# Kernel optimization log

Measured on AMD Instinct MI355X. Metric: run time of the kernel, lower is better.

## Reference

```python
import jax, jax.numpy as jnp
import numpy as np

B, S, IN_DIM, CTX = 32, 512, 256, 128
D, H, L = 128, 4, 2
DH = D // H
HID = 512
TOTAL = 11 * D * D + 8 * D  # hypernet flat weight size per sample
EPS = 1e-5


def _layernorm(x, g, b):
    mu = jnp.mean(x, axis=-1, keepdims=True)
    var = jnp.mean(jnp.square(x - mu), axis=-1, keepdims=True)
    return (x - mu) * jax.lax.rsqrt(var + EPS) * g + b


def setup_inputs() -> dict:
    key = jax.random.key(0)
    ks = jax.random.split(key, 24)
    f32 = jnp.float32
    inp = {
        'x': jax.random.normal(ks[0], (B, S, IN_DIM), f32),
        'context_vector': jax.random.normal(ks[1], (B, CTX), f32),
        'in_proj_w': jax.random.normal(ks[2], (D, IN_DIM), f32) * (IN_DIM ** -0.5),
        'in_proj_b': jnp.zeros((D,), f32),
        'pe': jax.random.normal(ks[3], (1, S, D), f32) * 0.02,
        'hfc1_w': jax.random.normal(ks[4], (L, HID, CTX), f32) * (CTX ** -0.5),
        'hfc1_b': jnp.zeros((L, HID), f32),
        'hfc2_w': jax.random.normal(ks[5], (L, TOTAL, HID), f32) * 0.02,
        'hfc2_b': jnp.zeros((L, TOTAL), f32),
        'out_proj_w': jax.random.normal(ks[6], (L, D, D), f32) * (D ** -0.5),
        'out_proj_b': jnp.zeros((L, D), f32),
        'ln1_g': jnp.ones((L, D), f32), 'ln1_b': jnp.zeros((L, D), f32),
        'ln2_g': jnp.ones((L, D), f32), 'ln2_b': jnp.zeros((L, D), f32),
        'alpha1': jnp.full((L,), 0.5, f32), 'alpha2': jnp.full((L,), 0.5, f32),
        'head_w': jax.random.normal(ks[7], (1, D), f32) * (D ** -0.5),
        'head_b': jnp.zeros((1,), f32),
    }
    return inp


def reference(x, context_vector, in_proj_w, in_proj_b, pe, hfc1_w, hfc1_b,
              hfc2_w, hfc2_b, out_proj_w, out_proj_b, ln1_g, ln1_b,
              ln2_g, ln2_b, alpha1, alpha2, head_w, head_b):
    # input projection + learned positional encoding
    h = jnp.einsum('bsi,di->bsd', x, in_proj_w) + in_proj_b
    h = h + pe[:, :h.shape[1], :]

    # flat split offsets for hypernet output
    sizes = [3 * D * D, 3 * D, 4 * D * D, 4 * D, 4 * D * D, D]
    offs = np.concatenate([[0], np.cumsum(sizes)])

    for l in range(L):
        # hypernet: per-sample weights from context
        hid = jax.nn.relu(context_vector @ hfc1_w[l].T + hfc1_b[l])
        flat = hid @ hfc2_w[l].T + hfc2_b[l]  # [B, TOTAL]
        aw = flat[:, offs[0]:offs[1]].reshape(B, 3 * D, D)
        ab = flat[:, offs[1]:offs[2]]                     # [B, 3D]
        f1w = flat[:, offs[2]:offs[3]].reshape(B, 4 * D, D)
        f1b = flat[:, offs[3]:offs[4]]                    # [B, 4D]
        f2w = flat[:, offs[4]:offs[5]].reshape(B, D, 4 * D)
        f2b = flat[:, offs[5]:offs[6]]                    # [B, D]

        # per-sample QKV projection (grouped GEMM over batch)
        qkv = jnp.einsum('bsd,bed->bse', h, aw) + ab[:, None, :]
        q, k, v = jnp.split(qkv, 3, axis=-1)
        q = q.reshape(B, S, H, DH)
        k = k.reshape(B, S, H, DH)
        v = v.reshape(B, S, H, DH)
        scores = jnp.einsum('bqhd,bkhd->bhqk', q, k) / jnp.sqrt(jnp.float32(DH))
        attn = jax.nn.softmax(scores, axis=-1)
        ctx = jnp.einsum('bhqk,bkhd->bqhd', attn, v).reshape(B, S, D)
        attn_out = jnp.einsum('bsd,ed->bse', ctx, out_proj_w[l]) + out_proj_b[l]

        h = _layernorm(h + alpha1[l] * attn_out, ln1_g[l], ln1_b[l])

        # per-sample FFN
        ff = jax.nn.relu(jnp.einsum('bsd,bfd->bsf', h, f1w) + f1b[:, None, :])
        ff = jnp.einsum('bsf,bdf->bsd', ff, f2w) + f2b[:, None, :]

        h = _layernorm(h + alpha2[l] * ff, ln2_g[l], ln2_b[l])

    out = h[:, -1, :] @ head_w.T + head_b  # [B, 1]
    return out
```

## Files before the change

kernel.cpp:

```cpp
#include <hip/hip_runtime.h>
#include <hip/hip_bf16.h>

constexpr int B_    = 32;
constexpr int S_    = 512;
constexpr int INDIM = 256;
constexpr int KCTX  = 128;
constexpr int D_    = 128;
constexpr int H_    = 4;
constexpr int L_    = 2;
constexpr int HID_  = 512;
constexpr int TOTAL_ = 11 * D_ * D_ + 8 * D_;
constexpr int OFF_AB  = 3 * D_ * D_;
constexpr int OFF_F1W = OFF_AB + 3 * D_;
constexpr int OFF_F1B = OFF_F1W + 4 * D_ * D_;
constexpr int OFF_F2W = OFF_F1B + 4 * D_;
constexpr int OFF_F2B = OFF_F2W + 4 * D_ * D_;
constexpr int TP = 132;

typedef __attribute__((ext_vector_type(8))) short short8;
typedef __attribute__((ext_vector_type(4))) short short4v;
typedef __attribute__((ext_vector_type(2))) short short2v;
typedef __attribute__((ext_vector_type(4))) float f32x4;

#define MFMA16 __builtin_amdgcn_mfma_f32_16x16x32_bf16

__device__ __forceinline__ short f2bf(float f) {
  __hip_bfloat16 h = __float2bfloat16(f);
  return __builtin_bit_cast(short, h);
}
__device__ __forceinline__ float bf2f(short s) {
  __hip_bfloat16 h = __builtin_bit_cast(__hip_bfloat16, s);
  return __bfloat162float(h);
}
struct bfpair { short hi, lo; };
__device__ __forceinline__ bfpair split2p(float x) {
  bfpair p;
  p.hi = f2bf(x);
  p.lo = f2bf(x - bf2f(p.hi));
  return p;
}

__device__ __forceinline__ void cvt_body(const float* __restrict__ in,
                                         short* __restrict__ oh,
                                         short* __restrict__ ol,
                                         int ktShift, int n8, int t) {
  if (t >= n8) return;
  int kt = 1 << ktShift;
  int row = t >> ktShift;
  int kc = t & (kt - 1);
  const float* p = in + ((long)row << (ktShift + 3)) + kc * 8;
  float4 v0 = *(const float4*)p;
  float4 v1 = *(const float4*)(p + 4);
  short8 h8, l8; bfpair q;
  q = split2p(v0.x); h8[0] = q.hi; l8[0] = q.lo;
  q = split2p(v0.y); h8[1] = q.hi; l8[1] = q.lo;
  q = split2p(v0.z); h8[2] = q.hi; l8[2] = q.lo;
  q = split2p(v0.w); h8[3] = q.hi; l8[3] = q.lo;
  q = split2p(v1.x); h8[4] = q.hi; l8[4] = q.lo;
  q = split2p(v1.y); h8[5] = q.hi; l8[5] = q.lo;
  q = split2p(v1.z); h8[6] = q.hi; l8[6] = q.lo;
  q = split2p(v1.w); h8[7] = q.hi; l8[7] = q.lo;
  long o = ((long)(row >> 4) * kt + kc) * 128 + (row & 15) * 8;
  *(short8*)(oh + o) = h8;
  *(short8*)(ol + o) = l8;
}

__global__ __launch_bounds__(256) void k_prep(
    const float* __restrict__ ipw, const float* __restrict__ opw,
    short* __restrict__ ipwFh, short* __restrict__ ipwFl,
    short* __restrict__ opwFh, short* __restrict__ opwFl,
    const float* __restrict__ cvec, const float* __restrict__ h1w,
    const float* __restrict__ h1b,
    short* __restrict__ hidFh, short* __restrict__ hidFl) {
  int id = blockIdx.x, tid = threadIdx.x;
  if (id < 16) {
    cvt_body(ipw, ipwFh, ipwFl, 5, D_ * INDIM / 8, id * 256 + tid);
  } else if (id < 32) {
    cvt_body(opw, opwFh, opwFl, 4, L_ * D_ * D_ / 8, (id - 16) * 256 + tid);
  } else {
    int hb = id - 32;
    int l = hb >> 5, b = hb & 31;
    __shared__ float cs[KCTX];
    if (tid < KCTX) cs[tid] = cvec[b * KCTX + tid];
    __syncthreads();
    #pragma unroll
    for (int jj = 0; jj < 2; ++jj) {
      int j = tid + jj * 256;
      const float* wr = h1w + (long)(l * HID_ + j) * KCTX;
      float s = h1b[l * HID_ + j];
      #pragma unroll
      for (int c = 0; c < KCTX; c += 4) {
        float4 cv = *(const float4*)(cs + c);
        float4 wv = *(const float4*)(wr + c);
        s += cv.x * wv.x + cv.y * wv.y + cv.z * wv.z + cv.w * wv.w;
      }
      s = fmaxf(s, 0.f);
      bfpair p = split2p(s);
      long o = (long)l * 32 * HID_ + ((long)(b >> 4) * 64 + (j >> 3)) * 128
             + (b & 15) * 8 + (j & 7);
      hidFh[o] = p.hi;
      hidFl[o] = p.lo;
    }
  }
}

__global__ __launch_bounds__(256) void k_flat_ip(
    const short* __restrict__ hidh, const short* __restrict__ hidl,
    const float* __restrict__ W, const float* __restrict__ bias,
    short* __restrict__ awh, short* __restrict__ awl,
    short* __restrict__ f1h, short* __restrict__ f1l,
    short* __restrict__ f2h, short* __restrict__ f2l,
    float* __restrict__ ab, float* __restrict__ f1b, float* __restrict__ f2b,
    const float* __restrict__ x,
    const short* __restrict__ ipwFh, const short* __restrict__ ipwFl,
    const float* __restrict__ ipb, const float* __restrict__ pe,
    float* __restrict__ h_f, short* __restrict__ hFh, short* __restrict__ hFl) {
  __shared__ short wls[2][2][64 * 64];
  const int id = blockIdx.x;
  const int tid = threadIdx.x, wave = tid >> 6, lane = tid & 63;
  const int r = lane & 15, g = lane >> 4;
  const int rr = tid >> 4;
  const int cc = (tid & 15) * 4;

  if (id < 256) {
    const int bx = id >> 5, b = id & 31;
    const float* abase = x + ((long)b * S_ + bx * 64) * INDIM;
    float4 av[2][4];
    #pragma unroll
    for (int rnd = 0; rnd < 4; ++rnd) {
      av[0][rnd] = *(const float4*)(abase + (long)(rnd * 16 + rr) * INDIM + cc);
      av[1][rnd] = *(const float4*)(abase + (long)(rnd * 16 + rr) * INDIM + 64 + cc);
    }
    const int n0 = (wave >> 1) * 64;
    const short* pWh = ipwFh + (n0 >> 4) * 4096 + g * 128 + r * 8;
    const short* pWl = ipwFl + (n0 >> 4) * 4096 + g * 128 + r * 8;
    f32x4 acc[2][4] = {{{0,0,0,0},{0,0,0,0},{0,0,0,0},{0,0,0,0}},
                       {{0,0,0,0},{0,0,0,0},{0,0,0,0},{0,0,0,0}}};
    for (int i = 0; i < 4; ++i) {
      int c0 = i * 64, cur = i & 1;
      #pragma unroll
      for (int rnd = 0; rnd < 4; ++rnd) {
        int row = rnd * 16 + rr;
        short4v h4, l4; bfpair q;
        q = split2p(av[cur][rnd].x); h4[0] = q.hi; l4[0] = q.lo;
        q = split2p(av[cur][rnd].y); h4[1] = q.hi; l4[1] = q.lo;
        q = split2p(av[cur][rnd].z); h4[2] = q.hi; l4[2] = q.lo;
        q = split2p(av[cur][rnd].w); h4[3] = q.hi; l4[3] = q.lo;
        int sb = row * 128 + ((cc * 2) ^ ((row & 7) << 4));
        *(short4v*)((char*)&wls[cur][0][0] + sb) = h4;
        *(short4v*)((char*)&wls[cur][1][0] + sb) = l4;
      }
      if (i + 2 < 4) {
        #pragma unroll
        for (int rnd = 0; rnd < 4; ++rnd)
          av[cur][rnd] = *(const float4*)(abase + (long)(rnd * 16 + rr) * INDIM + (c0 + 128) + cc);
      }
      __syncthreads();
      #pragma unroll
      for (int kk = 0; kk < 2; ++kk) {
        long wo = (long)(c0 * 16) + kk * 512;
        short8 ah[2], al[2];
        #pragma unroll
        for (int ms = 0; ms < 2; ++ms) {
          int arow = (wave & 1) * 32 + ms * 16 + r;
          int abyte = arow * 128 + ((kk * 64 + g * 16) ^ ((r & 7) << 4));
          ah[ms] = *(const short8*)((char*)&wls[cur][0][0] + abyte);
          al[ms] = *(const short8*)((char*)&wls[cur][1][0] + abyte);
        }
        #pragma unroll
        for (int ns = 0; ns < 4; ++ns) {
          short8 wh = *(const short8*)(pWh + ns * 4096 + wo);
          short8 wl = *(const short8*)(pWl + ns * 4096 + wo);
          #pragma unroll
          for (int ms = 0; ms < 2; ++ms) {
            acc[ms][ns] = MFMA16(ah[ms], wl, acc[ms][ns], 0, 0, 0);
            acc[ms][ns] = MFMA16(al[ms], wh, acc[ms][ns], 0, 0, 0);
            acc[ms][ns] = MFMA16(ah[ms], wh, acc[ms][ns], 0, 0, 0);
          }
        }
      }
      __syncthreads();
    }
    #pragma unroll
    for (int ms = 0; ms < 2; ++ms) {
      #pragma unroll
      for (int ns = 0; ns < 4; ++ns) {
        int ccol = n0 + ns * 16 + r;
        float bv = ipb[ccol];
        #pragma unroll
        for (int reg = 0; reg < 4; ++reg) {
          int crow = bx * 64 + (wave & 1) * 32 + ms * 16 + g * 4 + reg;
          float v = acc[ms][ns][reg] + bv + pe[crow * D_ + ccol];
          h_f[((long)b * S_ + crow) * D_ + ccol] = v;
          long o = (long)b * 65536 + (long)(crow >> 4) * 2048
                 + (ccol >> 3) * 128 + (crow & 15) * 8 + (ccol & 7);
          bfpair sp = split2p(v);
          hFh[o] = sp.hi;
          hFl[o] = sp.lo;
        }
      }
    }
    return;
  }

  const int fid = id - 256;
  const int l = fid / 2832;
  const int bxf = fid % 2832;
  hidh += (long)l * 32 * HID_;
  hidl += (long)l * 32 * HID_;
  W    += (long)l * TOTAL_ * HID_;
  bias += (long)l * TOTAL_;
  awh  += (long)l * B_ * 49152;  awl += (long)l * B_ * 49152;
  f1h  += (long)l * B_ * 65536;  f1l += (long)l * B_ * 65536;
  f2h  += (long)l * B_ * 65536;  f2l += (long)l * B_ * 65536;
  ab   += l * B_ * 384;  f1b += l * B_ * 512;  f2b += l * B_ * 128;
  const int nb0 = bxf * 64;
  const float* wbase = W + (long)nb0 * HID_;
  float4 wv[2][4];
  #pragma unroll
  for (int rnd = 0; rnd < 4; ++rnd) {
    wv[0][rnd] = *(const float4*)(wbase + (long)(rnd * 16 + rr) * HID_ + cc);
    wv[1][rnd] = *(const float4*)(wbase + (long)(rnd * 16 + rr) * HID_ + 64 + cc);
  }
  const short* pAh = hidh + g * 128 + r * 8;
  const short* pAl = hidl + g * 128 + r * 8;
  f32x4 acc0 = {0, 0, 0, 0}, acc1 = {0, 0, 0, 0};
  for (int i = 0; i < 8; ++i) {
    int c0 = i * 64, cur = i & 1;
    #pragma unroll
    for (int rnd = 0; rnd < 4; ++rnd) {
      int row = rnd * 16 + rr;
      short4v h4, l4; bfpair q;
      q = split2p(wv[cur][rnd].x); h4[0] = q.hi; l4[0] = q.lo;
      q = split2p(wv[cur][rnd].y); h4[1] = q.hi; l4[1] = q.lo;
      q = split2p(wv[cur][rnd].z); h4[2] = q.hi; l4[2] = q.lo;
      q = split2p(wv[cur][rnd].w); h4[3] = q.hi; l4[3] = q.lo;
      int sb = row * 128 + ((cc * 2) ^ ((row & 7) << 4));
      *(short4v*)((char*)&wls[cur][0][0] + sb) = h4;
      *(short4v*)((char*)&wls[cur][1][0] + sb) = l4;
    }
    if (i + 2 < 8) {
      #pragma unroll
      for (int rnd = 0; rnd < 4; ++rnd)
        wv[cur][rnd] = *(const float4*)(wbase + (long)(rnd * 16 + rr) * HID_ + (c0 + 128) + cc);
    }
    __syncthreads();
    #pragma unroll
    for (int kk = 0; kk < 2; ++kk) {
      long ao = (long)(c0 * 16) + kk * 512;
      short8 ah0 = *(const short8*)(pAh + ao);
      short8 ah1 = *(const short8*)(pAh + 8192 + ao);
      short8 al0 = *(const short8*)(pAl + ao);
      short8 al1 = *(const short8*)(pAl + 8192 + ao);
      int wrow = wave * 16 + r;
      int wb = wrow * 128 + ((kk * 64 + g * 16) ^ ((r & 7) << 4));
      short8 wh = *(const short8*)((char*)&wls[cur][0][0] + wb);
      short8 wl = *(const short8*)((char*)&wls[cur][1][0] + wb);
      acc0 = MFMA16(ah0, wl, acc0, 0, 0, 0);
      acc0 = MFMA16(al0, wh, acc0, 0, 0, 0);
      acc0 = MFMA16(ah0, wh, acc0, 0, 0, 0);
      acc1 = MFMA16(ah1, wl, acc1, 0, 0, 0);
      acc1 = MFMA16(al1, wh, acc1, 0, 0, 0);
      acc1 = MFMA16(ah1, wh, acc1, 0, 0, 0);
    }
    __syncthreads();
  }
  constexpr int TPF = 68;
  float* tile = (float*)&wls[0][0][0];
  {
    float bv = bias[nb0 + wave * 16 + r];
    int col = wave * 16 + r;
    #pragma unroll
    for (int reg = 0; reg < 4; ++reg) {
      tile[(g * 4 + reg) * TPF + col]      = acc0[reg] + bv;
      tile[(g * 4 + reg + 16) * TPF + col] = acc1[reg] + bv;
    }
  }
  __syncthreads();
  {
    int b  = tid >> 3;
    int cg = tid & 7;
    int t0 = nb0 + cg * 8;
    float v[8];
    #pragma unroll
    for (int j = 0; j < 8; ++j) v[j] = tile[b * TPF + cg * 8 + j];
    if (t0 < OFF_AB) {
      int e = t0 >> 7, d = t0 & 127;
      long a = (long)b * 49152 + ((long)(e >> 4) * 16 + (d >> 3)) * 128 + (e & 15) * 8;
      short8 h8, l8; bfpair q;
      #pragma unroll
      for (int j = 0; j < 8; ++j) { q = split2p(v[j]); h8[j] = q.hi; l8[j] = q.lo; }
      *(short8*)(awh + a) = h8;
      *(short8*)(awl + a) = l8;
    } else if (t0 < OFF_F1W) {
      float* dst = ab + b * 384 + (t0 - OFF_AB);
      float4 x0 = {v[0], v[1], v[2], v[3]}, x1 = {v[4], v[5], v[6], v[7]};
      *(float4*)dst = x0; *(float4*)(dst + 4) = x1;
    } else if (t0 < OFF_F1B) {
      int i = t0 - OFF_F1W; int f = i >> 7, d = i & 127;
      long a = (long)b * 65536 + ((long)(f >> 4) * 16 + (d >> 3)) * 128 + (f & 15) * 8;
      short8 h8, l8; bfpair q;
      #pragma unroll
      for (int j = 0; j < 8; ++j) { q = split2p(v[j]); h8[j] = q.hi; l8[j] = q.lo; }
      *(short8*)(f1h + a) = h8;
      *(short8*)(f1l + a) = l8;
    } else if (t0 < OFF_F2W) {
      float* dst = f1b + b * 512 + (t0 - OFF_F1B);
      float4 x0 = {v[0], v[1], v[2], v[3]}, x1 = {v[4], v[5], v[6], v[7]};
      *(float4*)dst = x0; *(float4*)(dst + 4) = x1;
    } else if (t0 < OFF_F2B) {
      int i = t0 - OFF_F2W; int dd = i >> 9, f = i & 511;
      long a = (long)b * 65536 + ((long)(dd >> 4) * 64 + (f >> 3)) * 128 + (dd & 15) * 8;
      short8 h8, l8; bfpair q;
      #pragma unroll
      for (int j = 0; j < 8; ++j) { q = split2p(v[j]); h8[j] = q.hi; l8[j] = q.lo; }
      *(short8*)(f2h + a) = h8;
      *(short8*)(f2l + a) = l8;
    } else {
      float* dst = f2b + b * 128 + (t0 - OFF_F2B);
      float4 x0 = {v[0], v[1], v[2], v[3]}, x1 = {v[4], v[5], v[6], v[7]};
      *(float4*)dst = x0; *(float4*)(dst + 4) = x1;
    }
  }
}

template <int K, int EPI, bool RELU>
__global__ __launch_bounds__(256) void k_gemm(
    const short* __restrict__ Ah, const short* __restrict__ Al, long sA,
    const short* __restrict__ Wh, const short* __restrict__ Wl, long sW,
    const float* __restrict__ biasP, long sB,
    void* __restrict__ p0, void* __restrict__ p1,
    void* __restrict__ p2, void* __restrict__ p3,
    int N,
    const float* __restrict__ lng, const float* __restrict__ lnb,
    const float* __restrict__ lnal, int mOff, int nOff, int mode) {
  extern __shared__ char smem_dyn[];
  const int tid = threadIdx.x, wave = tid >> 6, lane = tid & 63;
  const int r = lane & 15, g = lane >> 4;
  const int b = blockIdx.z;
  int bx, by;
  if (mode == 1) {
    int xx = blockIdx.x;
    if (xx < 16) { bx = xx >> 1; by = 1 + (xx & 1); }
    else         { bx = 7; by = 0; }
  } else {
    bx = blockIdx.x + mOff; by = blockIdx.y + nOff;
  }
  const int m0 = bx * 64 + (wave & 1) * 32;
  const int n0 = by * 128 + (wave >> 1) * 64;
  const long KT = (long)K * 16;
  const short* pAh = Ah + (long)b * sA + (m0 >> 4) * KT + g * 128 + r * 8;
  const short* pAl = Al + (long)b * sA + (m0 >> 4) * KT + g * 128 + r * 8;
  const short* pWh = Wh + (long)b * sW + (n0 >> 4) * KT + g * 128 + r * 8;
  const short* pWl = Wl + (long)b * sW + (n0 >> 4) * KT + g * 128 + r * 8;
  f32x4 acc[2][4] = {{{0,0,0,0},{0,0,0,0},{0,0,0,0},{0,0,0,0}},
                     {{0,0,0,0},{0,0,0,0},{0,0,0,0},{0,0,0,0}}};
  for (int kk = 0; kk < K / 32; ++kk) {
    long ko = (long)kk * 512;
    short8 a0h = *(const short8*)(pAh + ko);
    short8 a1h = *(const short8*)(pAh + KT + ko);
    short8 a0l = *(const short8*)(pAl + ko);
    short8 a1l = *(const short8*)(pAl + KT + ko);
    #pragma unroll
    for (int ns = 0; ns < 4; ++ns) {
      short8 wh = *(const short8*)(pWh + ns * KT + ko);
      short8 wl = *(const short8*)(pWl + ns * KT + ko);
      acc[0][ns] = MFMA16(a0h, wl, acc[0][ns], 0, 0, 0);
      acc[0][ns] = MFMA16(a0l, wh, acc[0][ns], 0, 0, 0);
      acc[0][ns] = MFMA16(a0h, wh, acc[0][ns], 0, 0, 0);
      acc[1][ns] = MFMA16(a1h, wl, acc[1][ns], 0, 0, 0);
      acc[1][ns] = MFMA16(a1l, wh, acc[1][ns], 0, 0, 0);
      acc[1][ns] = MFMA16(a1h, wh, acc[1][ns], 0, 0, 0);
    }
  }

  if constexpr (EPI == 5) {
    if (by == 2) {
      #pragma unroll
      for (int ms = 0; ms < 2; ++ms) {
        int crow0 = m0 + ms * 16 + g * 4;
        #pragma unroll
        for (int ns = 0; ns < 4; ++ns) {
          int ccol = n0 + ns * 16 + r;
          float bv = biasP[(long)b * sB + ccol];
          int c2 = ccol - 256, hd = c2 >> 5, dd = c2 & 31;
          short4v h4, l4; bfpair q;
          #pragma unroll
          for (int reg = 0; reg < 4; ++reg) {
            float v = acc[ms][ns][reg] + bv;
            q = split2p(v); h4[reg] = q.hi; l4[reg] = q.lo;
          }
          long o = (long)(b * 4 + hd) * 16384 + (dd >> 4) * 8192
                 + (crow0 >> 3) * 128 + (dd & 15) * 8 + (crow0 & 7);
          *(short4v*)((short*)p2 + o) = h4;
          *(short4v*)((short*)p3 + o) = l4;
        }
      }
      return;
    }
  }

  float* tile = (float*)smem_dyn;
  #pragma unroll
  for (int ms = 0; ms < 2; ++ms) {
    #pragma unroll
    for (int ns = 0; ns < 4; ++ns) {
      int ccol = n0 + ns * 16 + r;
      float bv = biasP[(long)b * sB + ccol];
      #pragma unroll
      for (int reg = 0; reg < 4; ++reg) {
        float v = acc[ms][ns][reg] + bv;
        if constexpr (RELU) v = fmaxf(v, 0.f);
        int trow2 = (wave & 1) * 32 + ms * 16 + g * 4 + reg;
        int tcol = (wave >> 1) * 64 + ns * 16 + r;
        tile[trow2 * TP + tcol] = v;
      }
    }
  }
  __syncthreads();

  if constexpr (EPI == 0 || EPI == 5) {
    int row = tid >> 2, cg = tid & 3;
    int crow = bx * 64 + row;
    long rowbase = (long)b * 512 * N + (long)(crow >> 4) * (16 * (long)N) + (crow & 15) * 8;
    #pragma unroll
    for (int j4 = 0; j4 < 4; ++j4) {
      int tcol = j4 * 32 + cg * 8;
      float4 aa = *(const float4*)&tile[row * TP + tcol];
      float4 bb = *(const float4*)&tile[row * TP + tcol + 4];
      short8 h8, l8; bfpair q;
      q = split2p(aa.x); h8[0] = q.hi; l8[0] = q.lo;
      q = split2p(aa.y); h8[1] = q.hi; l8[1] = q.lo;
      q = split2p(aa.z); h8[2] = q.hi; l8[2] = q.lo;
      q = split2p(aa.w); h8[3] = q.hi; l8[3] = q.lo;
      q = split2p(bb.x); h8[4] = q.hi; l8[4] = q.lo;
      q = split2p(bb.y); h8[5] = q.hi; l8[5] = q.lo;
      q = split2p(bb.z); h8[6] = q.hi; l8[6] = q.lo;
      q = split2p(bb.w); h8[7] = q.hi; l8[7] = q.lo;
      int ccol = by * 128 + tcol;
      long o = rowbase + (long)(ccol >> 3) * 128;
      *(short8*)((short*)p0 + o) = h8;
      *(short8*)((short*)p1 + o) = l8;
    }
  } else if constexpr (EPI == 4) {
    int row = tid >> 2, q = tid & 3;
    int brow = bx * 64 + row;
    float a = lnal[0];
    float* hf = (float*)p0;
    float* hrow = hf + ((long)b * S_ + brow) * D_ + q * 32;
    float tv[32];
    float s = 0.f, ss = 0.f;
    #pragma unroll
    for (int i = 0; i < 32; i += 4) {
      float4 hv = *(const float4*)(hrow + i);
      float4 yv = *(const float4*)&tile[row * TP + q * 32 + i];
      float t0 = hv.x + a * yv.x, t1 = hv.y + a * yv.y;
      float t2 = hv.z + a * yv.z, t3 = hv.w + a * yv.w;
      tv[i] = t0; tv[i+1] = t1; tv[i+2] = t2; tv[i+3] = t3;
      s += t0 + t1 + t2 + t3;
      ss += t0*t0 + t1*t1 + t2*t2 + t3*t3;
    }
    s  += __shfl_xor(s, 1);  s  += __shfl_xor(s, 2);
    ss += __shfl_xor(ss, 1); ss += __shfl_xor(ss, 2);
    float mu = s * (1.f / 128.f);
    float varv = ss * (1.f / 128.f) - mu * mu;
    float inv = rsqrtf(varv + 1e-5f);
    short* ph = (short*)p1; short* pl = (short*)p2;
    long fb = (long)b * 65536 + (long)(brow >> 4) * 2048 + (brow & 15) * 8;
    #pragma unroll
    for (int j = 0; j < 4; ++j) {
      short8 hv8, lv8;
      #pragma unroll
      for (int e = 0; e < 8; e += 4) {
        int i = j * 8 + e;
        int c = q * 32 + i;
        float4 gv = *(const float4*)(lng + c);
        float4 bb = *(const float4*)(lnb + c);
        float4 o4;
        o4.x = (tv[i]   - mu) * inv * gv.x + bb.x;
        o4.y = (tv[i+1] - mu) * inv * gv.y + bb.y;
        o4.z = (tv[i+2] - mu) * inv * gv.z + bb.z;
        o4.w = (tv[i+3] - mu) * inv * gv.w + bb.w;
        *(float4*)(hrow + i) = o4;
        bfpair q0 = split2p(o4.x); hv8[e]   = q0.hi; lv8[e]   = q0.lo;
        bfpair q1 = split2p(o4.y); hv8[e+1] = q1.hi; lv8[e+1] = q1.lo;
        bfpair q2 = split2p(o4.z); hv8[e+2] = q2.hi; lv8[e+2] = q2.lo;
        bfpair q3 = split2p(o4.w); hv8[e+3] = q3.hi; lv8[e+3] = q3.lo;
      }
      long o = fb + (q * 4 + j) * 128;
      *(short8*)(ph + o) = hv8;
      *(short8*)(pl + o) = lv8;
    }
  }
}

__global__ __launch_bounds__(128) void k_attn(const short* __restrict__ qkh,
                                              const short* __restrict__ qkl,
                                              const short* __restrict__ vth,
                                              const short* __restrict__ vtl,
                                              short* __restrict__ ch,
                                              short* __restrict__ cl,
                                              int mOff) {
  __shared__ __align__(16) float scr[16][516];
  __shared__ __align__(16) float obuf[16][34];
  const int tid = threadIdx.x, wave = tid >> 6, lane = tid & 63;
  const int r = lane & 15, g = lane >> 4;
  const int b = blockIdx.z, hh = blockIdx.y;
  const int m0 = (blockIdx.x + mOff) * 16;
  const long qb = (long)b * 131072;
  const long qoff = qb + (long)(m0 >> 4) * 4096 + (hh * 4 + g) * 128 + r * 8;
  short8 qh = *(const short8*)(qkh + qoff);
  short8 ql = *(const short8*)(qkl + qoff);
  const float sc = 0.17677669529663687f;
  for (int n0 = wave * 256; n0 < wave * 256 + 256; n0 += 16) {
    long koff = qb + (long)(n0 >> 4) * 4096 + (16 + hh * 4 + g) * 128 + r * 8;
    short8 kh = *(const short8*)(qkh + koff);
    short8 kl = *(const short8*)(qkl + koff);
    f32x4 s = {0, 0, 0, 0};
    s = MFMA16(qh, kl, s, 0, 0, 0);
    s = MFMA16(ql, kh, s, 0, 0, 0);
    s = MFMA16(qh, kh, s, 0, 0, 0);
    #pragma unroll
    for (int reg = 0; reg < 4; ++reg)
      scr[g * 4 + reg][n0 + r] = s[reg] * sc;
  }
  __syncthreads();
  for (int row = wave * 8; row < wave * 8 + 8; ++row) {
    float v[8];
    #pragma unroll
    for (int i = 0; i < 8; ++i) v[i] = scr[row][lane + i * 64];
    float m = v[0];
    #pragma unroll
    for (int i = 1; i < 8; ++i) m = fmaxf(m, v[i]);
    #pragma unroll
    for (int o = 32; o > 0; o >>= 1) m = fmaxf(m, __shfl_xor(m, o));
    float ssum = 0.f;
    #pragma unroll
    for (int i = 0; i < 8; ++i) { v[i] = __expf(v[i] - m); ssum += v[i]; }
    #pragma unroll
    for (int o = 32; o > 0; o >>= 1) ssum += __shfl_xor(ssum, o);
    float inv = 1.f / ssum;
    #pragma unroll
    for (int i = 0; i < 8; ++i) scr[row][lane + i * 64] = v[i] * inv;
  }
  __syncthreads();
  f32x4 o0 = {0, 0, 0, 0}, o1 = {0, 0, 0, 0};
  const long vb = (long)(b * 4 + hh) * 16384;
  for (int kt = wave * 8; kt < wave * 8 + 8; ++kt) {
    float4 pv0 = *(const float4*)&scr[r][kt * 32 + g * 8];
    float4 pv1 = *(const float4*)&scr[r][kt * 32 + g * 8 + 4];
    short8 pah, pal;
    bfpair p;
    p = split2p(pv0.x); pah[0] = p.hi; pal[0] = p.lo;
    p = split2p(pv0.y); pah[1] = p.hi; pal[1] = p.lo;
    p = split2p(pv0.z); pah[2] = p.hi; pal[2] = p.lo;
    p = split2p(pv0.w); pah[3] = p.hi; pal[3] = p.lo;
    p = split2p(pv1.x); pah[4] = p.hi; pal[4] = p.lo;
    p = split2p(pv1.y); pah[5] = p.hi; pal[5] = p.lo;
    p = split2p(pv1.z); pah[6] = p.hi; pal[6] = p.lo;
    p = split2p(pv1.w); pah[7] = p.hi; pal[7] = p.lo;
    long vo = vb + (long)(kt * 4 + g) * 128 + r * 8;
    short8 vh0 = *(const short8*)(vth + vo);
    short8 vh1 = *(const short8*)(vth + vo + 8192);
    short8 vl0 = *(const short8*)(vtl + vo);
    short8 vl1 = *(const short8*)(vtl + vo + 8192);
    o0 = MFMA16(pah, vl0, o0, 0, 0, 0);
    o0 = MFMA16(pal, vh0, o0, 0, 0, 0);
    o0 = MFMA16(pah, vh0, o0, 0, 0, 0);
    o1 = MFMA16(pah, vl1, o1, 0, 0, 0);
    o1 = MFMA16(pal, vh1, o1, 0, 0, 0);
    o1 = MFMA16(pah, vh1, o1, 0, 0, 0);
  }
  if (wave == 1) {
    #pragma unroll
    for (int reg = 0; reg < 4; ++reg) {
      obuf[g * 4 + reg][r] = o0[reg];
      obuf[g * 4 + reg][17 + r] = o1[reg];
    }
  }
  __syncthreads();
  if (wave == 0) {
    #pragma unroll
    for (int reg = 0; reg < 4; ++reg) {
      float a0 = o0[reg] + obuf[g * 4 + reg][r];
      float a1 = o1[reg] + obuf[g * 4 + reg][17 + r];
      int srow = m0 + g * 4 + reg;
      int col0 = hh * 32 + r;
      long o = (long)b * 65536 + (long)(srow >> 4) * 2048
             + (col0 >> 3) * 128 + (srow & 15) * 8 + (col0 & 7);
      bfpair sp0 = split2p(a0);
      ch[o] = sp0.hi; cl[o] = sp0.lo;
      long o2 = o + 2 * 128;
      bfpair sp1 = split2p(a1);
      ch[o2] = sp1.hi; cl[o2] = sp1.lo;
    }
  }
}

__global__ __launch_bounds__(64) void k_head(const float* __restrict__ h,
                                             const float* __restrict__ hw,
                                             const float* __restrict__ hb,
                                             float* __restrict__ out) {
  int b = blockIdx.x, lane = threadIdx.x;
  const float* hr = h + ((long)b * S_ + (S_ - 1)) * D_;
  float v = hr[lane] * hw[lane] + hr[lane + 64] * hw[lane + 64];
  #pragma unroll
  for (int o = 32; o > 0; o >>= 1) v += __shfl_xor(v, o);
  if (lane == 0) out[b] = v + hb[0];
}

extern "C" void kernel_launch(void* const* d_in, const int* in_sizes, int n_in,
                              void* d_out, int out_size, void* d_ws, size_t ws_size,
                              hipStream_t stream) {
  const float* x    = (const float*)d_in[0];
  const float* cvec = (const float*)d_in[1];
  const float* ipw  = (const float*)d_in[2];
  const float* ipb  = (const float*)d_in[3];
  const float* pe   = (const float*)d_in[4];
  const float* h1w  = (const float*)d_in[5];
  const float* h1b  = (const float*)d_in[6];
  const float* h2w  = (const float*)d_in[7];
  const float* h2b  = (const float*)d_in[8];
  const float* opw  = (const float*)d_in[9];
  const float* opb  = (const float*)d_in[10];
  const float* ln1g = (const float*)d_in[11];
  const float* ln1b = (const float*)d_in[12];
  const float* ln2g = (const float*)d_in[13];
  const float* ln2b = (const float*)d_in[14];
  const float* a1   = (const float*)d_in[15];
  const float* a2   = (const float*)d_in[16];
  const float* hw   = (const float*)d_in[17];
  const float* hb   = (const float*)d_in[18];
  float* out = (float*)d_out;

  char* ws = (char*)d_ws;
  size_t off = 0;
  auto alloc = [&](size_t n) { void* p = ws + off; off = (off + n + 255) & ~(size_t)255; return p; };

  const long AWs = (long)B_ * 49152;
  const long F1s = (long)B_ * 65536;
  const long F2s = (long)B_ * 65536;

  short* ff1h  = (short*)alloc((size_t)B_ * S_ * 512 * 2);
  short* ff1l  = (short*)alloc((size_t)B_ * S_ * 512 * 2);
  float* h_f   = (float*)alloc((size_t)B_ * S_ * D_ * 4);
  short* hFh   = (short*)alloc((size_t)B_ * S_ * D_ * 2);
  short* hFl   = (short*)alloc((size_t)B_ * S_ * D_ * 2);
  short* hidFh = (short*)alloc((size_t)L_ * 32 * HID_ * 2);
  short* hidFl = (short*)alloc((size_t)L_ * 32 * HID_ * 2);
  short* awFh  = (short*)alloc((size_t)L_ * AWs * 2);
  short* awFl  = (short*)alloc((size_t)L_ * AWs * 2);
  short* f1wFh = (short*)alloc((size_t)L_ * F1s * 2);
  short* f1wFl = (short*)alloc((size_t)L_ * F1s * 2);
  short* f2wFh = (short*)alloc((size_t)L_ * F2s * 2);
  short* f2wFl = (short*)alloc((size_t)L_ * F2s * 2);
  float* abF   = (float*)alloc((size_t)L_ * B_ * 384 * 4);
  float* f1bF  = (float*)alloc((size_t)L_ * B_ * 512 * 4);
  float* f2bF  = (float*)alloc((size_t)L_ * B_ * 128 * 4);
  short* qkFh  = (short*)alloc((size_t)B_ * S_ * 256 * 2);
  short* qkFl  = (short*)alloc((size_t)B_ * S_ * 256 * 2);
  short* vtFh  = (short*)alloc((size_t)B_ * H_ * 32 * S_ * 2);
  short* vtFl  = (short*)alloc((size_t)B_ * H_ * 32 * S_ * 2);
  short* cxFh  = (short*)alloc((size_t)B_ * S_ * D_ * 2);
  short* cxFl  = (short*)alloc((size_t)B_ * S_ * D_ * 2);
  short* ipwFh = (short*)alloc((size_t)D_ * INDIM * 2);
  short* ipwFl = (short*)alloc((size_t)D_ * INDIM * 2);
  short* opwFh = (short*)alloc((size_t)L_ * D_ * D_ * 2);
  short* opwFl = (short*)alloc((size_t)L_ * D_ * D_ * 2);

  k_prep<<<96, 256, 0, stream>>>(ipw, opw, ipwFh, ipwFl, opwFh, opwFl,
                                 cvec, h1w, h1b, hidFh, hidFl);

  k_flat_ip<<<256 + 2 * 2832, 256, 0, stream>>>(
      hidFh, hidFl, h2w, h2b, awFh, awFl, f1wFh, f1wFl, f2wFh, f2wFl,
      abF, f1bF, f2bF,
      x, ipwFh, ipwFl, ipb, pe, h_f, hFh, hFl);

  constexpr size_t TILE_LDS = 64 * TP * 4;

  {
    int l = 0;
    k_gemm<D_, 5, false><<<dim3(8, 3, B_), 256, TILE_LDS, stream>>>(
        hFh, hFl, (long)S_ * D_, awFh + l * AWs, awFl + l * AWs, 49152,
        abF + l * B_ * 384, 384,
        qkFh, qkFl, vtFh, vtFl, 256, nullptr, nullptr, nullptr, 0, 0, 0);
    k_attn<<<dim3(S_ / 16, H_, B_), 128, 0, stream>>>(qkFh, qkFl, vtFh, vtFl, cxFh, cxFl, 0);
    k_gemm<D_, 4, false><<<dim3(8, 1, B_), 256, TILE_LDS, stream>>>(
        cxFh, cxFl, (long)S_ * D_, opwFh + l * 16384, opwFl + l * 16384, 0,
        opb + l * D_, 0, h_f, hFh, hFl, nullptr, 128,
        ln1g + l * D_, ln1b + l * D_, a1 + l, 0, 0, 0);
    k_gemm<D_, 0, true><<<dim3(8, 4, B_), 256, TILE_LDS, stream>>>(
        hFh, hFl, (long)S_ * D_, f1wFh + l * F1s, f1wFl + l * F1s, 65536,
        f1bF + l * B_ * 512, 512,
        ff1h, ff1l, nullptr, nullptr, 512, nullptr, nullptr, nullptr, 0, 0, 0);
    k_gemm<512, 4, false><<<dim3(8, 1, B_), 256, TILE_LDS, stream>>>(
        ff1h, ff1l, (long)S_ * 512, f2wFh + l * F2s, f2wFl + l * F2s, 65536,
        f2bF + l * B_ * 128, 128,
        h_f, hFh, hFl, nullptr, 128,
        ln2g + l * D_, ln2b + l * D_, a2 + l, 0, 0, 0);
  }

  {
    int l = 1;
    k_gemm<D_, 5, false><<<dim3(17, 1, B_), 256, TILE_LDS, stream>>>(
        hFh, hFl, (long)S_ * D_, awFh + l * AWs, awFl + l * AWs, 49152,
        abF + l * B_ * 384, 384,
        qkFh, qkFl, vtFh, vtFl, 256, nullptr, nullptr, nullptr, 0, 0, 1);
    k_attn<<<dim3(1, H_, B_), 128, 0, stream>>>(qkFh, qkFl, vtFh, vtFl, cxFh, cxFl, 31);
    k_gemm<D_, 4, false><<<dim3(1, 1, B_), 256, TILE_LDS, stream>>>(
        cxFh, cxFl, (long)S_ * D_, opwFh + l * 16384, opwFl + l * 16384, 0,
        opb + l * D_, 0, h_f, hFh, hFl, nullptr, 128,
        ln1g + l * D_, ln1b + l * D_, a1 + l, 7, 0, 0);
    k_gemm<D_, 0, true><<<dim3(1, 4, B_), 256, TILE_LDS, stream>>>(
        hFh, hFl, (long)S_ * D_, f1wFh + l * F1s, f1wFl + l * F1s, 65536,
        f1bF + l * B_ * 512, 512,
        ff1h, ff1l, nullptr, nullptr, 512, nullptr, nullptr, nullptr, 7, 0, 0);
    k_gemm<512, 4, false><<<dim3(1, 1, B_), 256, TILE_LDS, stream>>>(
        ff1h, ff1l, (long)S_ * 512, f2wFh + l * F2s, f2wFl + l * F2s, 65536,
        f2bF + l * B_ * 128, 128,
        h_f, hFh, hFl, nullptr, 128,
        ln2g + l * D_, ln2b + l * D_, a2 + l, 7, 0, 0);
  }
  k_head<<<B_, 64, 0, stream>>>(h_f, hw, hb, out);
}
```

Before: 417.1 us.

## Fuse out-projection, residual layernorm and FFN1 GEMM into one kernel

Adds a k_opffn1 kernel that computes the attention out-projection, the residual plus layernorm, and then the first FFN GEMM with ReLU straight from the normalized tile held in LDS. This removes one kernel launch and the global round-trip of the normalized hidden state into the FFN1 GEMM. The price is that each of the 4 N-blocks (by) recomputes the out-projection and layernorm redundantly. The hidden state is ping-ponged between two buffers so blocks can read the old h while one of them writes the new one. The EPI==0 split-store path in k_gemm is dropped, and LDS base pointers are hoisted out of the inner loops.

```diff
diff --git a/kernel.cpp b/kernel.cpp
--- a/kernel.cpp
+++ b/kernel.cpp
@@ -138,6 +138,8 @@
                        {{0,0,0,0},{0,0,0,0},{0,0,0,0},{0,0,0,0}}};
     for (int i = 0; i < 4; ++i) {
       int c0 = i * 64, cur = i & 1;
+      char* bh = (char*)&wls[cur][0][0];
+      char* bl = (char*)&wls[cur][1][0];
       #pragma unroll
       for (int rnd = 0; rnd < 4; ++rnd) {
         int row = rnd * 16 + rr;
@@ -147,8 +149,8 @@
         q = split2p(av[cur][rnd].z); h4[2] = q.hi; l4[2] = q.lo;
         q = split2p(av[cur][rnd].w); h4[3] = q.hi; l4[3] = q.lo;
         int sb = row * 128 + ((cc * 2) ^ ((row & 7) << 4));
-        *(short4v*)((char*)&wls[cur][0][0] + sb) = h4;
-        *(short4v*)((char*)&wls[cur][1][0] + sb) = l4;
+        *(short4v*)(bh + sb) = h4;
+        *(short4v*)(bl + sb) = l4;
       }
       if (i + 2 < 4) {
         #pragma unroll
@@ -164,8 +166,8 @@
         for (int ms = 0; ms < 2; ++ms) {
           int arow = (wave & 1) * 32 + ms * 16 + r;
           int abyte = arow * 128 + ((kk * 64 + g * 16) ^ ((r & 7) << 4));
-          ah[ms] = *(const short8*)((char*)&wls[cur][0][0] + abyte);
-          al[ms] = *(const short8*)((char*)&wls[cur][1][0] + abyte);
+          ah[ms] = *(const short8*)(bh + abyte);
+          al[ms] = *(const short8*)(bl + abyte);
         }
         #pragma unroll
         for (int ns = 0; ns < 4; ++ns) {
@@ -227,6 +229,8 @@
   f32x4 acc0 = {0, 0, 0, 0}, acc1 = {0, 0, 0, 0};
   for (int i = 0; i < 8; ++i) {
     int c0 = i * 64, cur = i & 1;
+    char* bh = (char*)&wls[cur][0][0];
+    char* bl = (char*)&wls[cur][1][0];
     #pragma unroll
     for (int rnd = 0; rnd < 4; ++rnd) {
       int row = rnd * 16 + rr;
@@ -236,8 +240,8 @@
       q = split2p(wv[cur][rnd].z); h4[2] = q.hi; l4[2] = q.lo;
       q = split2p(wv[cur][rnd].w); h4[3] = q.hi; l4[3] = q.lo;
       int sb = row * 128 + ((cc * 2) ^ ((row & 7) << 4));
-      *(short4v*)((char*)&wls[cur][0][0] + sb) = h4;
-      *(short4v*)((char*)&wls[cur][1][0] + sb) = l4;
+      *(short4v*)(bh + sb) = h4;
+      *(short4v*)(bl + sb) = l4;
     }
     if (i + 2 < 8) {
       #pragma unroll
@@ -254,8 +258,8 @@
       short8 al1 = *(const short8*)(pAl + 8192 + ao);
       int wrow = wave * 16 + r;
       int wb = wrow * 128 + ((kk * 64 + g * 16) ^ ((r & 7) << 4));
-      short8 wh = *(const short8*)((char*)&wls[cur][0][0] + wb);
-      short8 wl = *(const short8*)((char*)&wls[cur][1][0] + wb);
+      short8 wh = *(const short8*)(bh + wb);
+      short8 wl = *(const short8*)(bl + wb);
       acc0 = MFMA16(ah0, wl, acc0, 0, 0, 0);
       acc0 = MFMA16(al0, wh, acc0, 0, 0, 0);
       acc0 = MFMA16(ah0, wh, acc0, 0, 0, 0);
@@ -419,7 +423,7 @@
   }
   __syncthreads();
 
-  if constexpr (EPI == 0 || EPI == 5) {
+  if constexpr (EPI == 5) {
     int row = tid >> 2, cg = tid & 3;
     int crow = bx * 64 + row;
     long rowbase = (long)b * 512 * N + (long)(crow >> 4) * (16 * (long)N) + (crow & 15) * 8;
@@ -490,6 +494,197 @@
       long o = fb + (q * 4 + j) * 128;
       *(short8*)(ph + o) = hv8;
       *(short8*)(pl + o) = lv8;
+    }
+  }
+}
+
+__global__ __launch_bounds__(256) void k_opffn1(
+    const short* __restrict__ cxh, const short* __restrict__ cxl,
+    const short* __restrict__ opwh, const short* __restrict__ opwl,
+    const float* __restrict__ opb,
+    const float* __restrict__ lng, const float* __restrict__ lnb,
+    const float* __restrict__ lnal,
+    const float* __restrict__ hfin, float* __restrict__ hfout,
+    short* __restrict__ hFh, short* __restrict__ hFl,
+    const short* __restrict__ f1wh, const short* __restrict__ f1wl,
+    const float* __restrict__ f1b,
+    short* __restrict__ ff1h, short* __restrict__ ff1l,
+    int mOff) {
+  __shared__ __align__(16) float tile[64 * TP];
+  const int tid = threadIdx.x, wave = tid >> 6, lane = tid & 63;
+  const int r = lane & 15, g = lane >> 4;
+  const int bx = blockIdx.x + mOff, by = blockIdx.y, b = blockIdx.z;
+  const int m0 = bx * 64 + (wave & 1) * 32;
+  {
+    const int n0 = (wave >> 1) * 64;
+    const short* pAh = cxh + (long)b * 65536 + (m0 >> 4) * 2048 + g * 128 + r * 8;
+    const short* pAl = cxl + (long)b * 65536 + (m0 >> 4) * 2048 + g * 128 + r * 8;
+    const short* pWh = opwh + (n0 >> 4) * 2048 + g * 128 + r * 8;
+    const short* pWl = opwl + (n0 >> 4) * 2048 + g * 128 + r * 8;
+    f32x4 acc[2][4] = {{{0,0,0,0},{0,0,0,0},{0,0,0,0},{0,0,0,0}},
+                       {{0,0,0,0},{0,0,0,0},{0,0,0,0},{0,0,0,0}}};
+    for (int kk = 0; kk < 4; ++kk) {
+      long ko = (long)kk * 512;
+      short8 a0h = *(const short8*)(pAh + ko);
+      short8 a1h = *(const short8*)(pAh + 2048 + ko);
+      short8 a0l = *(const short8*)(pAl + ko);
+      short8 a1l = *(const short8*)(pAl + 2048 + ko);
+      #pragma unroll
+      for (int ns = 0; ns < 4; ++ns) {
+        short8 wh = *(const short8*)(pWh + ns * 2048 + ko);
+        short8 wl = *(const short8*)(pWl + ns * 2048 + ko);
+        acc[0][ns] = MFMA16(a0h, wl, acc[0][ns], 0, 0, 0);
+        acc[0][ns] = MFMA16(a0l, wh, acc[0][ns], 0, 0, 0);
+        acc[0][ns] = MFMA16(a0h, wh, acc[0][ns], 0, 0, 0);
+        acc[1][ns] = MFMA16(a1h, wl, acc[1][ns], 0, 0, 0);
+        acc[1][ns] = MFMA16(a1l, wh, acc[1][ns], 0, 0, 0);
+        acc[1][ns] = MFMA16(a1h, wh, acc[1][ns], 0, 0, 0);
+      }
+    }
+    #pragma unroll
+    for (int ms = 0; ms < 2; ++ms) {
+      #pragma unroll
+      for (int ns = 0; ns < 4; ++ns) {
+        int ccol = n0 + ns * 16 + r;
+        float bv = opb[ccol];
+        #pragma unroll
+        for (int reg = 0; reg < 4; ++reg) {
+          int trow2 = (wave & 1) * 32 + ms * 16 + g * 4 + reg;
+          tile[trow2 * TP + ccol] = acc[ms][ns][reg] + bv;
+        }
+      }
+    }
+  }
+  __syncthreads();
+  {
+    int row = tid >> 2, q = tid & 3;
+    int brow = bx * 64 + row;
+    float a = lnal[0];
+    const float* hrowIn = hfin + ((long)b * S_ + brow) * D_ + q * 32;
+    float tv[32];
+    float s = 0.f, ss = 0.f;
+    #pragma unroll
+    for (int i = 0; i < 32; i += 4) {
+      float4 hv = *(const float4*)(hrowIn + i);
+      float4 yv = *(const float4*)&tile[row * TP + q * 32 + i];
+      float t0 = hv.x + a * yv.x, t1 = hv.y + a * yv.y;
+      float t2 = hv.z + a * yv.z, t3 = hv.w + a * yv.w;
+      tv[i] = t0; tv[i+1] = t1; tv[i+2] = t2; tv[i+3] = t3;
+      s += t0 + t1 + t2 + t3;
+      ss += t0*t0 + t1*t1 + t2*t2 + t3*t3;
+    }
+    s  += __shfl_xor(s, 1);  s  += __shfl_xor(s, 2);
+    ss += __shfl_xor(ss, 1); ss += __shfl_xor(ss, 2);
+    float mu = s * (1.f / 128.f);
+    float varv = ss * (1.f / 128.f) - mu * mu;
+    float inv = rsqrtf(varv + 1e-5f);
+    float* hrowOut = hfout + ((long)b * S_ + brow) * D_ + q * 32;
+    long fb = (long)b * 65536 + (long)(brow >> 4) * 2048 + (brow & 15) * 8;
+    #pragma unroll
+    for (int j = 0; j < 4; ++j) {
+      short8 hv8, lv8;
+      #pragma unroll
+      for (int e = 0; e < 8; e += 4) {
+        int i = j * 8 + e;
+        int c = q * 32 + i;
+        float4 gv = *(const float4*)(lng + c);
+        float4 bb = *(const float4*)(lnb + c);
+        float4 o4;
+        o4.x = (tv[i]   - mu) * inv * gv.x + bb.x;
+        o4.y = (tv[i+1] - mu) * inv * gv.y + bb.y;
+        o4.z = (tv[i+2] - mu) * inv * gv.z + bb.z;
+        o4.w = (tv[i+3] - mu) * inv * gv.w + bb.w;
+        *(float4*)&tile[row * TP + c] = o4;
+        if (by == 0) *(float4*)(hrowOut + i) = o4;
+        bfpair q0 = split2p(o4.x); hv8[e]   = q0.hi; lv8[e]   = q0.lo;
+        bfpair q1 = split2p(o4.y); hv8[e+1] = q1.hi; lv8[e+1] = q1.lo;
+        bfpair q2 = split2p(o4.z); hv8[e+2] = q2.hi; lv8[e+2] = q2.lo;
+        bfpair q3 = split2p(o4.w); hv8[e+3] = q3.hi; lv8[e+3] = q3.lo;
+      }
+      if (by == 0) {
+        long o = fb + (q * 4 + j) * 128;
+        *(short8*)(hFh + o) = hv8;
+        *(short8*)(hFl + o) = lv8;
+      }
+    }
+  }
+  __syncthreads();
+  const int n1 = by * 128 + (wave >> 1) * 64;
+  f32x4 acc2[2][4] = {{{0,0,0,0},{0,0,0,0},{0,0,0,0},{0,0,0,0}},
+                      {{0,0,0,0},{0,0,0,0},{0,0,0,0},{0,0,0,0}}};
+  {
+    const short* qWh = f1wh + (long)b * 65536 + (n1 >> 4) * 2048 + g * 128 + r * 8;
+    const short* qWl = f1wl + (long)b * 65536 + (n1 >> 4) * 2048 + g * 128 + r * 8;
+    for (int kk = 0; kk < 4; ++kk) {
+      short8 ah[2], al[2];
+      #pragma unroll
+      for (int ms = 0; ms < 2; ++ms) {
+        int arow = (wave & 1) * 32 + ms * 16 + r;
+        float4 a0 = *(const float4*)&tile[arow * TP + kk * 32 + g * 8];
+        float4 a1 = *(const float4*)&tile[arow * TP + kk * 32 + g * 8 + 4];
+        bfpair q;
+        q = split2p(a0.x); ah[ms][0] = q.hi; al[ms][0] = q.lo;
+        q = split2p(a0.y); ah[ms][1] = q.hi; al[ms][1] = q.lo;
+        q = split2p(a0.z); ah[ms][2] = q.hi; al[ms][2] = q.lo;
+        q = split2p(a0.w); ah[ms][3] = q.hi; al[ms][3] = q.lo;
+        q = split2p(a1.x); ah[ms][4] = q.hi; al[ms][4] = q.lo;
+        q = split2p(a1.y); ah[ms][5] = q.hi; al[ms][5] = q.lo;
+        q = split2p(a1.z); ah[ms][6] = q.hi; al[ms][6] = q.lo;
+        q = split2p(a1.w); ah[ms][7] = q.hi; al[ms][7] = q.lo;
+      }
+      long ko = (long)kk * 512;
+      #pragma unroll
+      for (int ns = 0; ns < 4; ++ns) {
+        short8 wh = *(const short8*)(qWh + ns * 2048 + ko);
+        short8 wl = *(const short8*)(qWl + ns * 2048 + ko);
+        #pragma unroll
+        for (int ms = 0; ms < 2; ++ms) {
+          acc2[ms][ns] = MFMA16(ah[ms], wl, acc2[ms][ns], 0, 0, 0);
+          acc2[ms][ns] = MFMA16(al[ms], wh, acc2[ms][ns], 0, 0, 0);
+          acc2[ms][ns] = MFMA16(ah[ms], wh, acc2[ms][ns], 0, 0, 0);
+        }
+      }
+    }
+  }
+  __syncthreads();
+  #pragma unroll
+  for (int ms = 0; ms < 2; ++ms) {
+    #pragma unroll
+    for (int ns = 0; ns < 4; ++ns) {
+      int ccol = n1 + ns * 16 + r;
+      float bv = f1b[(long)b * 512 + ccol];
+      #pragma unroll
+      for (int reg = 0; reg < 4; ++reg) {
+        float v = fmaxf(acc2[ms][ns][reg] + bv, 0.f);
+        int trow2 = (wave & 1) * 32 + ms * 16 + g * 4 + reg;
+        int tcol = (wave >> 1) * 64 + ns * 16 + r;
+        tile[trow2 * TP + tcol] = v;
+      }
+    }
+  }
+  __syncthreads();
+  {
+    int row = tid >> 2, cg = tid & 3;
+    int crow = bx * 64 + row;
+    long rowbase = (long)b * 512 * 512 + (long)(crow >> 4) * (16 * 512) + (crow & 15) * 8;
+    #pragma unroll
+    for (int j4 = 0; j4 < 4; ++j4) {
+      int tcol = j4 * 32 + cg * 8;
+      float4 aa = *(const float4*)&tile[row * TP + tcol];
+      float4 bb = *(const float4*)&tile[row * TP + tcol + 4];
+      short8 h8, l8; bfpair q;
+      q = split2p(aa.x); h8[0] = q.hi; l8[0] = q.lo;
+      q = split2p(aa.y); h8[1] = q.hi; l8[1] = q.lo;
+      q = split2p(aa.z); h8[2] = q.hi; l8[2] = q.lo;
+      q = split2p(aa.w); h8[3] = q.hi; l8[3] = q.lo;
+      q = split2p(bb.x); h8[4] = q.hi; l8[4] = q.lo;
+      q = split2p(bb.y); h8[5] = q.hi; l8[5] = q.lo;
+      q = split2p(bb.z); h8[6] = q.hi; l8[6] = q.lo;
+      q = split2p(bb.w); h8[7] = q.hi; l8[7] = q.lo;
+      int ccol = by * 128 + tcol;
+      long o = rowbase + (long)(ccol >> 3) * 128;
+      *(short8*)(ff1h + o) = h8;
+      *(short8*)(ff1l + o) = l8;
     }
   }
 }
@@ -643,7 +838,8 @@
 
   short* ff1h  = (short*)alloc((size_t)B_ * S_ * 512 * 2);
   short* ff1l  = (short*)alloc((size_t)B_ * S_ * 512 * 2);
-  float* h_f   = (float*)alloc((size_t)B_ * S_ * D_ * 4);
+  float* h_fA  = (float*)alloc((size_t)B_ * S_ * D_ * 4);
+  float* h_fB  = (float*)alloc((size_t)B_ * S_ * D_ * 4);
   short* hFh   = (short*)alloc((size_t)B_ * S_ * D_ * 2);
   short* hFl   = (short*)alloc((size_t)B_ * S_ * D_ * 2);
   short* hidFh = (short*)alloc((size_t)L_ * 32 * HID_ * 2);
@@ -674,7 +870,7 @@
   k_flat_ip<<<256 + 2 * 2832, 256, 0, stream>>>(
       hidFh, hidFl, h2w, h2b, awFh, awFl, f1wFh, f1wFl, f2wFh, f2wFl,
       abF, f1bF, f2bF,
-      x, ipwFh, ipwFl, ipb, pe, h_f, hFh, hFl);
+      x, ipwFh, ipwFl, ipb, pe, h_fA, hFh, hFl);
 
   constexpr size_t TILE_LDS = 64 * TP * 4;
 
@@ -685,18 +881,16 @@
         abF + l * B_ * 384, 384,
         qkFh, qkFl, vtFh, vtFl, 256, nullptr, nullptr, nullptr, 0, 0, 0);
     k_attn<<<dim3(S_ / 16, H_, B_), 128, 0, stream>>>(qkFh, qkFl, vtFh, vtFl, cxFh, cxFl, 0);
-    k_gemm<D_, 4, false><<<dim3(8, 1, B_), 256, TILE_LDS, stream>>>(
-        cxFh, cxFl, (long)S_ * D_, opwFh + l * 16384, opwFl + l * 16384, 0,
-        opb + l * D_, 0, h_f, hFh, hFl, nullptr, 128,
-        ln1g + l * D_, ln1b + l * D_, a1 + l, 0, 0, 0);
-    k_gemm<D_, 0, true><<<dim3(8, 4, B_), 256, TILE_LDS, stream>>>(
-        hFh, hFl, (long)S_ * D_, f1wFh + l * F1s, f1wFl + l * F1s, 65536,
-        f1bF + l * B_ * 512, 512,
-        ff1h, ff1l, nullptr, nullptr, 512, nullptr, nullptr, nullptr, 0, 0, 0);
+    k_opffn1<<<dim3(8, 4, B_), 256, 0, stream>>>(
+        cxFh, cxFl, opwFh + l * 16384, opwFl + l * 16384, opb + l * D_,
+        ln1g + l * D_, ln1b + l * D_, a1 + l,
+        h_fA, h_fB, hFh, hFl,
+        f1wFh + l * F1s, f1wFl + l * F1s, f1bF + l * B_ * 512,
+        ff1h, ff1l, 0);
     k_gemm<512, 4, false><<<dim3(8, 1, B_), 256, TILE_LDS, stream>>>(
         ff1h, ff1l, (long)S_ * 512, f2wFh + l * F2s, f2wFl + l * F2s, 65536,
         f2bF + l * B_ * 128, 128,
-        h_f, hFh, hFl, nullptr, 128,
+        h_fB, hFh, hFl, nullptr, 128,
         ln2g + l * D_, ln2b + l * D_, a2 + l, 0, 0, 0);
   }
 
@@ -707,19 +901,17 @@
         abF + l * B_ * 384, 384,
         qkFh, qkFl, vtFh, vtFl, 256, nullptr, nullptr, nullptr, 0, 0, 1);
     k_attn<<<dim3(1, H_, B_), 128, 0, stream>>>(qkFh, qkFl, vtFh, vtFl, cxFh, cxFl, 31);
-    k_gemm<D_, 4, false><<<dim3(1, 1, B_), 256, TILE_LDS, stream>>>(
-        cxFh, cxFl, (long)S_ * D_, opwFh + l * 16384, opwFl + l * 16384, 0,
-        opb + l * D_, 0, h_f, hFh, hFl, nullptr, 128,
-        ln1g + l * D_, ln1b + l * D_, a1 + l, 7, 0, 0);
-    k_gemm<D_, 0, true><<<dim3(1, 4, B_), 256, TILE_LDS, stream>>>(
-        hFh, hFl, (long)S_ * D_, f1wFh + l * F1s, f1wFl + l * F1s, 65536,
-        f1bF + l * B_ * 512, 512,
-        ff1h, ff1l, nullptr, nullptr, 512, nullptr, nullptr, nullptr, 7, 0, 0);
+    k_opffn1<<<dim3(1, 4, B_), 256, 0, stream>>>(
+        cxFh, cxFl, opwFh + l * 16384, opwFl + l * 16384, opb + l * D_,
+        ln1g + l * D_, ln1b + l * D_, a1 + l,
+        h_fB, h_fA, hFh, hFl,
+        f1wFh + l * F1s, f1wFl + l * F1s, f1bF + l * B_ * 512,
+        ff1h, ff1l, 7);
     k_gemm<512, 4, false><<<dim3(1, 1, B_), 256, TILE_LDS, stream>>>(
         ff1h, ff1l, (long)S_ * 512, f2wFh + l * F2s, f2wFl + l * F2s, 65536,
         f2bF + l * B_ * 128, 128,
-        h_f, hFh, hFl, nullptr, 128,
+        h_fA, hFh, hFl, nullptr, 128,
         ln2g + l * D_, ln2b + l * D_, a2 + l, 7, 0, 0);
   }
-  k_head<<<B_, 64, 0, stream>>>(h_f, hw, hb, out);
-}
+  k_head<<<B_, 64, 0, stream>>>(h_fA, hw, hb, out);
+}
```

New measurement: 417.1 us (median of 2 runs). Within noise of the previous version (+0.0%).
